# Performance work log

Measured on AMD Instinct MI355X. Metric: run time of the kernel, lower is better.

## Reference

```python
import jax, jax.numpy as jnp
import numpy as np

B, T, E, NH, NLEV = 16, 2048, 1024, 16, 12
HD = E // NH


def _level_matrix(length):
    # Vectorized version of get_level_index_weak (base=2): levels[t, s] for s < t.
    tt, ss = np.meshgrid(np.arange(length), np.arange(length), indexing='ij')
    t = tt.copy(); s = ss.copy()
    lev = np.zeros((length, length), dtype=np.int32)
    active = tt > ss
    while active.any():
        l = np.floor(np.log2(np.maximum(t, 1))).astype(np.int64)
        v = (1 << l)
        done = active & (s < v)
        lev[done] = (l[done] + 1).astype(np.int32)
        cont = active & ~done
        t = np.where(cont, t - v, t)
        s = np.where(cont, s - v, s)
        active = cont
    return lev  # lev[t,t] = 0 (diagonal uses level 0)


def setup_inputs() -> dict:
    key = jax.random.key(0)
    ks = jax.random.split(key, 12)
    s = 0.02
    inp = {
        'x': jax.random.normal(ks[0], (B, T, E), jnp.float32),
        'Wq': jax.random.normal(ks[1], (E, E), jnp.float32) * s,
        'bq': jnp.zeros((E,), jnp.float32),
        'Wk': jax.random.normal(ks[2], (E, E), jnp.float32) * s,
        'bk': jnp.zeros((E,), jnp.float32),
        'Wv': jax.random.normal(ks[3], (E, E), jnp.float32) * s,
        'bv': jnp.zeros((E,), jnp.float32),
        'A_log': jax.random.normal(ks[4], (T, NH), jnp.float32),
        'A_bias': jnp.zeros((T, NH), jnp.float32),
        'L': jax.random.normal(ks[5], (T, NH, NLEV), jnp.float32),
        'L_bias': jnp.zeros((T, NH, NLEV), jnp.float32),
        'Wo': jax.random.normal(ks[6], (E, E), jnp.float32) * s,
        'bo': jnp.zeros((E,), jnp.float32),
        'levels': jnp.asarray(_level_matrix(T)),
    }
    return inp


def reference(x, Wq, bq, Wk, bk, Wv, bv, A_log, A_bias, L, L_bias, Wo, bo, levels):
    Bn, Tn, En = x.shape
    NHh = A_log.shape[1]
    HDd = En // NHh
    # q/k projections exist in the original forward but are never used by the
    # hierarchical attention; keep only v (q/k are dead code -> omitted).
    v = (x @ Wv.T + bv).reshape(Bn, Tn, NHh, HDd).transpose(0, 2, 1, 3)  # [B,H,T,D]

    # Decay factors: prod(A[s+1:t+1]) == exp(cumsum(logA)[t] - cumsum(logA)[s]).
    A = jax.nn.sigmoid(A_log + A_bias)            # [T, H]
    cs = jnp.cumsum(jnp.log(A), axis=0)           # [T, H]
    decay = jnp.exp(cs[:, None, :] - cs[None, :, :])  # [t, s, H]; diag == 1

    # Hierarchical level weights: G[t, s, h] = (L + L_bias)[t, h, levels[t, s]].
    Le = L + L_bias                               # [T, H, NLEV]
    G = Le[jnp.arange(Tn)[:, None], :, levels]    # [t, s, H]

    causal = jnp.tril(jnp.ones((Tn, Tn), dtype=bool))[:, :, None]
    Hm = jnp.where(causal, G * decay, jnp.zeros((), x.dtype))  # [t, s, H]

    # Original softmaxes the full row (upper triangle is 0, not -inf) -> keep that.
    attn = jax.nn.softmax(Hm, axis=1)             # over source dim s
    out = jnp.einsum('tsh,bhsd->bhtd', attn, v)   # [B,H,T,D]
    out = out.transpose(0, 2, 1, 3).reshape(Bn, Tn, En)
    return out @ Wo.T + bo
```

## Files before the change

kernel.cpp:

```cpp
#include <hip/hip_runtime.h>
#include <stdint.h>

static constexpr int Bn = 16, Tn = 2048, En = 1024, NHn = 16, HDn = 64, NLEVn = 12;

typedef __attribute__((ext_vector_type(8))) short short8;
typedef __attribute__((ext_vector_type(4))) float floatx4;

__device__ __forceinline__ unsigned short f2bf(float f) {
  unsigned int u = __float_as_uint(f);
  u += 0x7fffu + ((u >> 16) & 1u);
  return (unsigned short)(u >> 16);
}
__device__ __forceinline__ float bf2f(unsigned short s) {
  return __uint_as_float(((unsigned int)s) << 16);
}

__device__ __forceinline__ void async16(const unsigned short* g, unsigned short* l) {
  __builtin_amdgcn_global_load_lds(
      (const __attribute__((address_space(1))) unsigned int*)g,
      (__attribute__((address_space(3))) unsigned int*)l, 16, 0, 0);
}

__global__ void k_cvt(const float* __restrict__ in, unsigned short* __restrict__ out, int n4) {
  int i = blockIdx.x * 256 + threadIdx.x;
  if (i < n4) {
    float4 v = ((const float4*)in)[i];
    ushort4 o;
    o.x = f2bf(v.x); o.y = f2bf(v.y); o.z = f2bf(v.z); o.w = f2bf(v.w);
    ((ushort4*)out)[i] = o;
  }
}

__global__ void k_scan(const float* __restrict__ A_log, const float* __restrict__ A_bias,
                       float* __restrict__ cs) {
  int h = blockIdx.x;
  int tid = threadIdx.x;
  __shared__ float part[256];
  float loc[8];
  float run = 0.f;
#pragma unroll
  for (int j = 0; j < 8; j++) {
    int t = tid * 8 + j;
    float x = A_log[t * NHn + h] + A_bias[t * NHn + h];
    float ls = -log1pf(__expf(-x));
    run += ls;
    loc[j] = run;
  }
  part[tid] = run;
  __syncthreads();
  for (int d = 1; d < 256; d <<= 1) {
    float v = (tid >= d) ? part[tid - d] : 0.f;
    __syncthreads();
    part[tid] += v;
    __syncthreads();
  }
  float off = (tid > 0) ? part[tid - 1] : 0.f;
#pragma unroll
  for (int j = 0; j < 8; j++) cs[(tid * 8 + j) * NHn + h] = loc[j] + off;
}

__global__ void k_weights(const float* __restrict__ L, const float* __restrict__ Lb,
                          const int* __restrict__ levels, const float* __restrict__ cs,
                          unsigned short* __restrict__ P, float* __restrict__ denom) {
  int t = blockIdx.x;
  int tid = threadIdx.x;
  __shared__ float Lrow[NHn * NLEVn];
  __shared__ float cst[NHn];
  __shared__ float dsum[NHn];
  if (tid < NHn * NLEVn) Lrow[tid] = L[t * NHn * NLEVn + tid] + Lb[t * NHn * NLEVn + tid];
  if (tid < NHn) { cst[tid] = cs[t * NHn + tid]; dsum[tid] = 0.f; }
  __syncthreads();
  float acc[NHn];
#pragma unroll
  for (int h = 0; h < NHn; h++) acc[h] = 0.f;
  for (int s = tid; s < Tn; s += 256) {
    int lev = levels[(size_t)t * Tn + s];
    bool causal = (s <= t);
    float csr[NHn];
    const float4* c4 = (const float4*)(cs + s * NHn);
#pragma unroll
    for (int q = 0; q < 4; q++) {
      float4 v = c4[q];
      csr[q * 4 + 0] = v.x; csr[q * 4 + 1] = v.y; csr[q * 4 + 2] = v.z; csr[q * 4 + 3] = v.w;
    }
#pragma unroll
    for (int h = 0; h < NHn; h++) {
      float w = 1.f;
      if (causal) {
        float dec = __expf(cst[h] - csr[h]);
        w = __expf(Lrow[h * NLEVn + lev] * dec);
      }
      unsigned short pb = f2bf(w);
      acc[h] += bf2f(pb);
      P[((size_t)h * Tn + t) * Tn + s] = pb;
    }
  }
  int lane = tid & 63;
#pragma unroll
  for (int h = 0; h < NHn; h++) {
    float v = acc[h];
    for (int o = 32; o > 0; o >>= 1) v += __shfl_down(v, o, 64);
    if (lane == 0) atomicAdd(&dsum[h], v);
  }
  __syncthreads();
  if (tid < NHn) denom[(size_t)tid * Tn + t] = dsum[tid];
}

__global__ __launch_bounds__(512)
void k_gemm_v(const unsigned short* __restrict__ A, const unsigned short* __restrict__ Bm,
              const float* __restrict__ bias, unsigned short* __restrict__ vt) {
  __shared__ unsigned short smem[24576];
  unsigned short* As = smem;
  unsigned short* Bs = smem + 16384;
  const int K = 1024;
  int tid = threadIdx.x;
  int wave = tid >> 6, lane = tid & 63;
  int wm = wave >> 1, wn = wave & 1;

  int flat = blockIdx.y * 8 + blockIdx.x;
  int xcd = flat & 7, slot = flat >> 3;
  int strip = xcd * 16 + (slot >> 3);
  int nt = slot & 7;
  int bm = strip * 256, bn = nt * 128;

  floatx4 zero4 = {0.f, 0.f, 0.f, 0.f};
  floatx4 acc[4][4];
#pragma unroll
  for (int i = 0; i < 4; i++)
#pragma unroll
    for (int j = 0; j < 4; j++) acc[i][j] = zero4;

  for (int k0 = 0; k0 < K; k0 += 64) {
    __syncthreads();
#pragma unroll
    for (int j = 0; j < 4; j++) {
      int f = j * 512 + tid;
      int r = f >> 3, c = f & 7;
      int cg = c ^ (r & 7);
      async16(&A[(size_t)(bm + r) * K + k0 + cg * 8], &As[f * 8]);
    }
#pragma unroll
    for (int j = 0; j < 2; j++) {
      int f = j * 512 + tid;
      int r = f >> 3, c = f & 7;
      int cg = c ^ (r & 7);
      async16(&Bm[(size_t)(bn + r) * K + k0 + cg * 8], &Bs[f * 8]);
    }
    __syncthreads();
#pragma unroll
    for (int kk = 0; kk < 2; kk++) {
      short8 af[4], bfr[4];
      int cgk = kk * 4 + (lane >> 4);
#pragma unroll
      for (int i = 0; i < 4; i++) {
        int m = wm * 64 + i * 16 + (lane & 15);
        af[i] = *(const short8*)&As[m * 64 + ((cgk ^ (m & 7)) * 8)];
        int n = wn * 64 + i * 16 + (lane & 15);
        bfr[i] = *(const short8*)&Bs[n * 64 + ((cgk ^ (n & 7)) * 8)];
      }
#pragma unroll
      for (int i = 0; i < 4; i++)
#pragma unroll
        for (int j = 0; j < 4; j++)
          acc[i][j] = __builtin_amdgcn_mfma_f32_16x16x32_bf16(af[i], bfr[j], acc[i][j], 0, 0, 0);
    }
  }

  int b = bm >> 11, t0 = bm & 2047;
  unsigned short* Ct = smem;
  const int S = 264;
#pragma unroll 1
  for (int pass = 0; pass < 2; pass++) {
    __syncthreads();
    if (wn == pass) {
#pragma unroll
      for (int i = 0; i < 4; i++) {
#pragma unroll
        for (int j = 0; j < 4; j++) {
          int colL = j * 16 + (lane & 15);
          float bia = bias[bn + pass * 64 + colL];
          int rowb = wm * 64 + i * 16 + (lane >> 4) * 4;
          ushort4 p;
          p.x = f2bf(acc[i][j][0] + bia);
          p.y = f2bf(acc[i][j][1] + bia);
          p.z = f2bf(acc[i][j][2] + bia);
          p.w = f2bf(acc[i][j][3] + bia);
          *(ushort4*)&Ct[colL * S + rowb] = p;
        }
      }
    }
    __syncthreads();
#pragma unroll
    for (int cc = 0; cc < 4; cc++) {
      int colL = wave * 8 + cc * 2 + (lane >> 5);
      int gc = bn + pass * 64 + colL;
      int h = gc >> 6, d = gc & 63;
      int tt = (lane & 31) * 8;
      short8 v = *(const short8*)&Ct[colL * S + tt];
      *(short8*)&vt[((size_t)((h * Bn + b) * HDn + d)) * Tn + t0 + tt] = v;
    }
  }
}


#define STAGE_A(kt, half, buf)                                                   \
  {                                                                              \
    _Pragma("unroll")                                                            \
    for (int j_ = 0; j_ < 2; j_++) {                                             \
      int f_ = j_ * 512 + tid;                                                   \
      int r_ = f_ >> 3, c_ = f_ & 7;                                             \
      int cg_ = c_ ^ (r_ & 7);                                                   \
      async16(&Ap[(size_t)(bm + (half) * 128 + r_) * K + (kt) * 64 + cg_ * 8],   \
              &smem[(buf) * 32768 + ((half) * 128 + r_) * 64 + c_ * 8]);         \
    }                                                                            \
  }

#define STAGE_B(kt, half, buf)                                                   \
  {                                                                              \
    _Pragma("unroll")                                                            \
    for (int j_ = 0; j_ < 2; j_++) {                                             \
      int f_ = j_ * 512 + tid;                                                   \
      int r_ = f_ >> 3, c_ = f_ & 7;                                             \
      int cg_ = c_ ^ (r_ & 7);                                                   \
      async16(&Bp[(size_t)(bn + (half) * 128 + r_) * K + (kt) * 64 + cg_ * 8],   \
              &smem[(buf) * 32768 + 16384 + ((half) * 128 + r_) * 64 + c_ * 8]); \
    }                                                                            \
  }

#define LOAD_A(buf, Mh)                                                          \
  {                                                                              \
    _Pragma("unroll")                                                            \
    for (int ii_ = 0; ii_ < 4; ii_++) {                                          \
      int m_ = (Mh) * 128 + wm * 64 + ii_ * 16 + (lane & 15);                    \
      _Pragma("unroll")                                                          \
      for (int kk_ = 0; kk_ < 2; kk_++) {                                        \
        int cgk_ = kk_ * 4 + (lane >> 4);                                        \
        aR[ii_][kk_] =                                                           \
            *(const short8*)&smem[(buf) * 32768 + m_ * 64 + ((cgk_ ^ (m_ & 7)) * 8)]; \
      }                                                                          \
    }                                                                            \
  }

#define LOAD_B(buf, Nh)                                                          \
  {                                                                              \
    _Pragma("unroll")                                                            \
    for (int jj_ = 0; jj_ < 2; jj_++) {                                          \
      int n_ = (Nh) * 128 + wn * 32 + jj_ * 16 + (lane & 15);                    \
      _Pragma("unroll")                                                          \
      for (int kk_ = 0; kk_ < 2; kk_++) {                                        \
        int cgk_ = kk_ * 4 + (lane >> 4);                                        \
        bR[jj_][kk_] = *(const short8*)&smem[(buf) * 32768 + 16384 + n_ * 64 +   \
                                             ((cgk_ ^ (n_ & 7)) * 8)];           \
      }                                                                          \
    }                                                                            \
  }

#define MFMA16(Mh, Nh)                                                           \
  {                                                                              \
    __builtin_amdgcn_s_setprio(1);                                               \
    _Pragma("unroll")                                                            \
    for (int kk_ = 0; kk_ < 2; kk_++)                                            \
      _Pragma("unroll")                                                          \
      for (int ii_ = 0; ii_ < 4; ii_++)                                          \
        _Pragma("unroll")                                                        \
        for (int jj_ = 0; jj_ < 2; jj_++)                                        \
          acc[(Mh) * 4 + ii_][(Nh) * 2 + jj_] = __builtin_amdgcn_mfma_f32_16x16x32_bf16( \
              aR[ii_][kk_], bR[jj_][kk_], acc[(Mh) * 4 + ii_][(Nh) * 2 + jj_], 0, 0, 0); \
    __builtin_amdgcn_s_setprio(0);                                               \
  }

#define WAIT6 asm volatile("s_waitcnt vmcnt(6)" ::: "memory")
#define BAR                                                                      \
  {                                                                              \
    asm volatile("" ::: "memory");                                               \
    __builtin_amdgcn_s_barrier();                                                \
    asm volatile("" ::: "memory");                                               \
  }

__global__ __launch_bounds__(512, 2)
void k_gemm_attn(const unsigned short* __restrict__ P, const unsigned short* __restrict__ vt,
                 const float* __restrict__ denom, unsigned short* __restrict__ outp) {
  __shared__ unsigned short smem[65536];
  const int K = Tn;
  int tid = threadIdx.x;
  int wave = tid >> 6, lane = tid & 63;
  int wm = wave >> 2, wn = wave & 3;

  int flat = blockIdx.y * 8 + blockIdx.x;
  int wg = (flat & 7) * 64 + (flat >> 3);
  int h = wg >> 5;
  int mt = (wg >> 2) & 7, nt = wg & 3;
  int bm = mt * 256, bn = nt * 256;

  const unsigned short* Ap = P + (size_t)h * Tn * Tn;
  const unsigned short* Bp = vt + (size_t)h * (Bn * HDn) * Tn;

  floatx4 zero4 = {0.f, 0.f, 0.f, 0.f};
  floatx4 acc[8][4];
#pragma unroll
  for (int i = 0; i < 8; i++)
#pragma unroll
    for (int j = 0; j < 4; j++) acc[i][j] = zero4;

  short8 aR[4][2], bR[2][2];

  STAGE_A(0, 0, 0);
  STAGE_B(0, 0, 0);
  STAGE_B(0, 1, 0);
  STAGE_A(0, 1, 0);

  const int nk = K / 64;
  for (int t = 0; t < nk; t++) {
    int buf = t & 1, nbuf = buf ^ 1;
    int tn = (t < nk - 1) ? t + 1 : nk - 1;

    STAGE_A(tn, 0, nbuf);
    WAIT6; BAR;
    LOAD_A(buf, 0);
    LOAD_B(buf, 0);
    MFMA16(0, 0);
    BAR;
    STAGE_B(tn, 0, nbuf);
    WAIT6; BAR;
    LOAD_B(buf, 1);
    MFMA16(0, 1);
    BAR;
    STAGE_B(tn, 1, nbuf);
    WAIT6; BAR;
    LOAD_A(buf, 1);
    MFMA16(1, 1);
    BAR;
    STAGE_A(tn, 1, nbuf);
    WAIT6; BAR;
    LOAD_B(buf, 0);
    MFMA16(1, 0);
    BAR;
  }
  asm volatile("s_waitcnt vmcnt(0)" ::: "memory");

#pragma unroll
  for (int i = 0; i < 8; i++) {
    int rb = bm + (i >> 2) * 128 + wm * 64 + (i & 3) * 16 + (lane >> 4) * 4;
#pragma unroll
    for (int r = 0; r < 4; r++) {
      int row = rb + r;
      float sc = 1.f / denom[(size_t)h * Tn + row];
#pragma unroll
      for (int j = 0; j < 4; j++) {
        int col = bn + (j >> 1) * 128 + wn * 32 + (j & 1) * 16 + (lane & 15);
        int b = col >> 6, d = col & 63;
        outp[((size_t)(b * Tn + row)) * En + h * HDn + d] = f2bf(acc[i][j][r] * sc);
      }
    }
  }
}

__global__ __launch_bounds__(256)
void k_gemm_out(const unsigned short* __restrict__ A, const unsigned short* __restrict__ Bm,
                const float* __restrict__ bias, float* __restrict__ out) {
  __shared__ unsigned short As[128 * 64];
  __shared__ unsigned short Bs[128 * 64];
  const int K = 1024, N = 1024;
  int tid = threadIdx.x;
  int wave = tid >> 6, lane = tid & 63;
  int wm = wave >> 1, wn = wave & 1;

  int flat = blockIdx.y * 8 + blockIdx.x;
  int xcd = flat & 7, slot = flat >> 3;
  int strip = xcd * 32 + (slot >> 3);
  int nt = slot & 7;
  int bm = strip * 128, bn = nt * 128;

  floatx4 zero4 = {0.f, 0.f, 0.f, 0.f};
  floatx4 acc[4][4];
#pragma unroll
  for (int i = 0; i < 4; i++)
#pragma unroll
    for (int j = 0; j < 4; j++) acc[i][j] = zero4;

  for (int k0 = 0; k0 < K; k0 += 64) {
    __syncthreads();
#pragma unroll
    for (int j = 0; j < 4; j++) {
      int f = j * 256 + tid;
      int r = f >> 3, c = f & 7;
      int cg = c ^ (r & 7);
      async16(&A[(size_t)(bm + r) * K + k0 + cg * 8], &As[f * 8]);
    }
#pragma unroll
    for (int j = 0; j < 4; j++) {
      int f = j * 256 + tid;
      int r = f >> 3, c = f & 7;
      int cg = c ^ (r & 7);
      async16(&Bm[(size_t)(bn + r) * K + k0 + cg * 8], &Bs[f * 8]);
    }
    __syncthreads();
#pragma unroll
    for (int kk = 0; kk < 2; kk++) {
      short8 af[4], bfr[4];
      int cgk = kk * 4 + (lane >> 4);
#pragma unroll
      for (int i = 0; i < 4; i++) {
        int m = wm * 64 + i * 16 + (lane & 15);
        af[i] = *(const short8*)&As[m * 64 + ((cgk ^ (m & 7)) * 8)];
        int n = wn * 64 + i * 16 + (lane & 15);
        bfr[i] = *(const short8*)&Bs[n * 64 + ((cgk ^ (n & 7)) * 8)];
      }
#pragma unroll
      for (int i = 0; i < 4; i++)
#pragma unroll
        for (int j = 0; j < 4; j++)
          acc[i][j] = __builtin_amdgcn_mfma_f32_16x16x32_bf16(af[i], bfr[j], acc[i][j], 0, 0, 0);
    }
  }
#pragma unroll
  for (int i = 0; i < 4; i++) {
#pragma unroll
    for (int j = 0; j < 4; j++) {
#pragma unroll
      for (int r = 0; r < 4; r++) {
        int row = bm + wm * 64 + i * 16 + (lane >> 4) * 4 + r;
        int col = bn + wn * 64 + j * 16 + (lane & 15);
        out[(size_t)row * N + col] = acc[i][j][r] + bias[col];
      }
    }
  }
}

extern "C" void kernel_launch(void* const* d_in, const int* in_sizes, int n_in,
                              void* d_out, int out_size, void* d_ws, size_t ws_size,
                              hipStream_t stream) {
  const float* x      = (const float*)d_in[0];
  const float* Wv     = (const float*)d_in[5];
  const float* bv     = (const float*)d_in[6];
  const float* A_log  = (const float*)d_in[7];
  const float* A_bias = (const float*)d_in[8];
  const float* L      = (const float*)d_in[9];
  const float* Lb     = (const float*)d_in[10];
  const float* Wo     = (const float*)d_in[11];
  const float* bo     = (const float*)d_in[12];
  const int* levels   = (const int*)d_in[13];
  float* out = (float*)d_out;

  char* ws = (char*)d_ws;
  float* cs            = (float*)(ws + 0);
  float* denom         = (float*)(ws + 131072);
  unsigned short* Wvb  = (unsigned short*)(ws + 262144);
  unsigned short* Wob  = (unsigned short*)(ws + 2359296);
  unsigned short* xb   = (unsigned short*)(ws + 4456448);
  unsigned short* Pw   = (unsigned short*)(ws + 4456448);
  unsigned short* vt   = (unsigned short*)(ws + 138674176);
  unsigned short* outp = (unsigned short*)(ws + 205783040);
  if (ws_size < 272891904ULL) return;

  int nx4 = Bn * Tn * En / 4;
  k_cvt<<<(nx4 + 255) / 256, 256, 0, stream>>>(x, xb, nx4);
  int nw4 = En * En / 4;
  k_cvt<<<(nw4 + 255) / 256, 256, 0, stream>>>(Wv, Wvb, nw4);
  k_cvt<<<(nw4 + 255) / 256, 256, 0, stream>>>(Wo, Wob, nw4);
  k_scan<<<NHn, 256, 0, stream>>>(A_log, A_bias, cs);

  k_gemm_v<<<dim3(8, 128), 512, 0, stream>>>(xb, Wvb, bv, vt);

  k_weights<<<Tn, 256, 0, stream>>>(L, Lb, levels, cs, Pw, denom);

  k_gemm_attn<<<dim3(8, 64), 512, 0, stream>>>(Pw, vt, denom, outp);

  k_gemm_out<<<dim3(8, 256), 256, 0, stream>>>(outp, Wob, bo, out);
}
```

Baseline: 634.6 us.

## Restructure attention GEMM k-loop and port output GEMM to 256x256 pipelined tile

New measurement: 618.6 us. -2.5%, faster.

```diff
diff --git a/kernel.cpp b/kernel.cpp
--- a/kernel.cpp
+++ b/kernel.cpp
@@ -249,8 +249,8 @@
       _Pragma("unroll")                                                          \
       for (int kk_ = 0; kk_ < 2; kk_++) {                                        \
         int cgk_ = kk_ * 4 + (lane >> 4);                                        \
-        bR[jj_][kk_] = *(const short8*)&smem[(buf) * 32768 + 16384 + n_ * 64 +   \
-                                             ((cgk_ ^ (n_ & 7)) * 8)];           \
+        bR[Nh][jj_][kk_] = *(const short8*)&smem[(buf) * 32768 + 16384 + n_ * 64 + \
+                                                 ((cgk_ ^ (n_ & 7)) * 8)];       \
       }                                                                          \
     }                                                                            \
   }
@@ -265,16 +265,34 @@
         _Pragma("unroll")                                                        \
         for (int jj_ = 0; jj_ < 2; jj_++)                                        \
           acc[(Mh) * 4 + ii_][(Nh) * 2 + jj_] = __builtin_amdgcn_mfma_f32_16x16x32_bf16( \
-              aR[ii_][kk_], bR[jj_][kk_], acc[(Mh) * 4 + ii_][(Nh) * 2 + jj_], 0, 0, 0); \
+              aR[ii_][kk_], bR[Nh][jj_][kk_], acc[(Mh) * 4 + ii_][(Nh) * 2 + jj_], 0, 0, 0); \
     __builtin_amdgcn_s_setprio(0);                                               \
   }
 
-#define WAIT6 asm volatile("s_waitcnt vmcnt(6)" ::: "memory")
+#define WAIT8 asm volatile("s_waitcnt vmcnt(8)" ::: "memory")
 #define BAR                                                                      \
   {                                                                              \
     asm volatile("" ::: "memory");                                               \
     __builtin_amdgcn_s_barrier();                                                \
     asm volatile("" ::: "memory");                                               \
+  }
+
+#define KTILE_BODY(buf, nbuf, tn)                                                \
+  {                                                                              \
+    STAGE_A(tn, 0, nbuf);                                                        \
+    STAGE_B(tn, 0, nbuf);                                                        \
+    STAGE_B(tn, 1, nbuf);                                                        \
+    STAGE_A(tn, 1, nbuf);                                                        \
+    WAIT8; BAR;                                                                  \
+    LOAD_A(buf, 0);                                                              \
+    LOAD_B(buf, 0);                                                              \
+    LOAD_B(buf, 1);                                                              \
+    MFMA16(0, 0);                                                                \
+    MFMA16(0, 1);                                                                \
+    LOAD_A(buf, 1);                                                              \
+    MFMA16(1, 1);                                                                \
+    MFMA16(1, 0);                                                                \
+    BAR;                                                                         \
   }
 
 __global__ __launch_bounds__(512, 2)
@@ -302,7 +320,7 @@
 #pragma unroll
     for (int j = 0; j < 4; j++) acc[i][j] = zero4;
 
-  short8 aR[4][2], bR[2][2];
+  short8 aR[4][2], bR[2][2][2];
 
   STAGE_A(0, 0, 0);
   STAGE_B(0, 0, 0);
@@ -313,28 +331,7 @@
   for (int t = 0; t < nk; t++) {
     int buf = t & 1, nbuf = buf ^ 1;
     int tn = (t < nk - 1) ? t + 1 : nk - 1;
-
-    STAGE_A(tn, 0, nbuf);
-    WAIT6; BAR;
-    LOAD_A(buf, 0);
-    LOAD_B(buf, 0);
-    MFMA16(0, 0);
-    BAR;
-    STAGE_B(tn, 0, nbuf);
-    WAIT6; BAR;
-    LOAD_B(buf, 1);
-    MFMA16(0, 1);
-    BAR;
-    STAGE_B(tn, 1, nbuf);
-    WAIT6; BAR;
-    LOAD_A(buf, 1);
-    MFMA16(1, 1);
-    BAR;
-    STAGE_A(tn, 1, nbuf);
-    WAIT6; BAR;
-    LOAD_B(buf, 0);
-    MFMA16(1, 0);
-    BAR;
+    KTILE_BODY(buf, nbuf, tn);
   }
   asm volatile("s_waitcnt vmcnt(0)" ::: "memory");
 
@@ -355,72 +352,54 @@
   }
 }
 
-__global__ __launch_bounds__(256)
+__global__ __launch_bounds__(512, 2)
 void k_gemm_out(const unsigned short* __restrict__ A, const unsigned short* __restrict__ Bm,
                 const float* __restrict__ bias, float* __restrict__ out) {
-  __shared__ unsigned short As[128 * 64];
-  __shared__ unsigned short Bs[128 * 64];
+  __shared__ unsigned short smem[65536];
   const int K = 1024, N = 1024;
   int tid = threadIdx.x;
   int wave = tid >> 6, lane = tid & 63;
-  int wm = wave >> 1, wn = wave & 1;
+  int wm = wave >> 2, wn = wave & 3;
 
   int flat = blockIdx.y * 8 + blockIdx.x;
-  int xcd = flat & 7, slot = flat >> 3;
-  int strip = xcd * 32 + (slot >> 3);
-  int nt = slot & 7;
-  int bm = strip * 128, bn = nt * 128;
+  int wg = (flat & 7) * 64 + (flat >> 3);
+  int mt = wg >> 2, nt = wg & 3;
+  int bm = mt * 256, bn = nt * 256;
+
+  const unsigned short* Ap = A;
+  const unsigned short* Bp = Bm;
 
   floatx4 zero4 = {0.f, 0.f, 0.f, 0.f};
-  floatx4 acc[4][4];
-#pragma unroll
-  for (int i = 0; i < 4; i++)
+  floatx4 acc[8][4];
+#pragma unroll
+  for (int i = 0; i < 8; i++)
 #pragma unroll
     for (int j = 0; j < 4; j++) acc[i][j] = zero4;
 
-  for (int k0 = 0; k0 < K; k0 += 64) {
-    __syncthreads();
-#pragma unroll
-    for (int j = 0; j < 4; j++) {
-      int f = j * 256 + tid;
-      int r = f >> 3, c = f & 7;
-      int cg = c ^ (r & 7);
-      async16(&A[(size_t)(bm + r) * K + k0 + cg * 8], &As[f * 8]);
-    }
-#pragma unroll
-    for (int j = 0; j < 4; j++) {
-      int f = j * 256 + tid;
-      int r = f >> 3, c = f & 7;
-      int cg = c ^ (r & 7);
-      async16(&Bm[(size_t)(bn + r) * K + k0 + cg * 8], &Bs[f * 8]);
-    }
-    __syncthreads();
-#pragma unroll
-    for (int kk = 0; kk < 2; kk++) {
-      short8 af[4], bfr[4];
-      int cgk = kk * 4 + (lane >> 4);
-#pragma unroll
-      for (int i = 0; i < 4; i++) {
-        int m = wm * 64 + i * 16 + (lane & 15);
-        af[i] = *(const short8*)&As[m * 64 + ((cgk ^ (m & 7)) * 8)];
-        int n = wn * 64 + i * 16 + (lane & 15);
-        bfr[i] = *(const short8*)&Bs[n * 64 + ((cgk ^ (n & 7)) * 8)];
-      }
-#pragma unroll
-      for (int i = 0; i < 4; i++)
-#pragma unroll
-        for (int j = 0; j < 4; j++)
-          acc[i][j] = __builtin_amdgcn_mfma_f32_16x16x32_bf16(af[i], bfr[j], acc[i][j], 0, 0, 0);
-    }
-  }
-#pragma unroll
-  for (int i = 0; i < 4; i++) {
-#pragma unroll
-    for (int j = 0; j < 4; j++) {
-#pragma unroll
-      for (int r = 0; r < 4; r++) {
-        int row = bm + wm * 64 + i * 16 + (lane >> 4) * 4 + r;
-        int col = bn + wn * 64 + j * 16 + (lane & 15);
+  short8 aR[4][2], bR[2][2][2];
+
+  STAGE_A(0, 0, 0);
+  STAGE_B(0, 0, 0);
+  STAGE_B(0, 1, 0);
+  STAGE_A(0, 1, 0);
+
+  const int nk = K / 64;
+  for (int t = 0; t < nk; t++) {
+    int buf = t & 1, nbuf = buf ^ 1;
+    int tn = (t < nk - 1) ? t + 1 : nk - 1;
+    KTILE_BODY(buf, nbuf, tn);
+  }
+  asm volatile("s_waitcnt vmcnt(0)" ::: "memory");
+
+#pragma unroll
+  for (int i = 0; i < 8; i++) {
+    int rb = bm + (i >> 2) * 128 + wm * 64 + (i & 3) * 16 + (lane >> 4) * 4;
+#pragma unroll
+    for (int r = 0; r < 4; r++) {
+      int row = rb + r;
+#pragma unroll
+      for (int j = 0; j < 4; j++) {
+        int col = bn + (j >> 1) * 128 + wn * 32 + (j & 1) * 16 + (lane & 15);
         out[(size_t)row * N + col] = acc[i][j][r] + bias[col];
       }
     }
@@ -466,5 +445,5 @@
 
   k_gemm_attn<<<dim3(8, 64), 512, 0, stream>>>(Pw, vt, denom, outp);
 
-  k_gemm_out<<<dim3(8, 256), 256, 0, stream>>>(outp, Wob, bo, out);
-}
+  k_gemm_out<<<dim3(8, 64), 512, 0, stream>>>(outp, Wob, bo, out);
+}
```
